# Kernel optimization log

Hardware: AMD Instinct MI355X
Metric: run time of the kernel (lower is better)

Reference implementation:

```python
import jax, jax.numpy as jnp
import numpy as np

EPS = 1e-5

def setup_inputs() -> dict:
    key = jax.random.key(0)
    ks = jax.random.split(key, 5)
    B, C, N, L = 32, 128, 4096, 6
    M = N // 8  # 512
    x = jax.random.normal(ks[0], (B, C, N, 1), dtype=jnp.float32)
    # small init scale keeps softmax logits in a sane range
    W_pool = jax.random.normal(ks[1], (M, C), dtype=jnp.float32) * 0.05
    Wf = jax.random.normal(ks[2], (L, M, M), dtype=jnp.float32) * 0.02
    gamma = jnp.ones((L, M), dtype=jnp.float32)
    beta = jnp.zeros((L, M), dtype=jnp.float32)
    W_unpool = jax.random.normal(ks[3], (M, C), dtype=jnp.float32) * 0.05
    b_unpool = jnp.zeros((M,), dtype=jnp.float32)
    return {"x": x, "W_pool": W_pool, "Wf": Wf, "gamma": gamma,
            "beta": beta, "W_unpool": W_unpool, "b_unpool": b_unpool}


def reference(x, W_pool, Wf, gamma, beta, W_unpool, b_unpool):
    # x: [B, C, N, 1]
    xs = x[..., 0]  # [B, C, N]
    # ---- Pool_1_to_1: 1x1 conv C->M, softmax over N, weighted sum ----
    Spool = jax.nn.softmax(jnp.einsum('mc,bcn->bmn', W_pool, xs), axis=2)
    h = jnp.einsum('bcn,bmn->bmc', xs, Spool)  # pooled then transposed: [B, M, C]
    # ---- n_layers of Order_Aware_Filtering_1_to_1 on [B, M, C] (channels=M) ----
    L = Wf.shape[0]
    for l in range(L):
        y = jnp.einsum('om,bmc->boc', Wf[l], h)  # 1x1 conv M->M
        mu = jnp.mean(y, axis=(0, 2), keepdims=True)          # BN over (B, spatial)
        var = jnp.mean((y - mu) ** 2, axis=(0, 2), keepdims=True)  # biased var
        yn = (y - mu) * jax.lax.rsqrt(var + EPS)
        yn = yn * gamma[l][None, :, None] + beta[l][None, :, None]
        h = jax.nn.relu(yn + h)  # residual + non-lin
    x1 = jnp.transpose(h, (0, 2, 1))  # [B, C, M]
    # ---- Unpool_1_to_1: 1x1 conv (with bias) C->M, softmax over M ----
    ul = jnp.einsum('mc,bcn->bmn', W_unpool, xs) + b_unpool[None, :, None]
    Sun = jax.nn.softmax(ul, axis=1)
    out = jnp.einsum('bcm,bmn->bcn', x1, Sun)
    return out[..., None]  # [B, C, N, 1]
```

## Files before the change

### kernel.cpp

```cpp
#include <hip/hip_runtime.h>
#include <hip/hip_bf16.h>

typedef float f32x4 __attribute__((ext_vector_type(4)));
typedef __bf16 bf16_t;
typedef __bf16 bf16x4 __attribute__((ext_vector_type(4)));
typedef __bf16 bf16x8 __attribute__((ext_vector_type(8)));

#define MFMA16(a, b, c) __builtin_amdgcn_mfma_f32_16x16x32_bf16(a, b, c, 0, 0, 0)

constexpr int C_ = 128;
constexpr int N_ = 4096;
constexpr int M_ = 512;
constexpr int NL = 6;

#define NEG_INF (-__builtin_huge_valf())

constexpr int XST = 136;
constexpr int NSTP = 40;
constexpr int PSTU = 72;

__global__ __launch_bounds__(256) void k_wsplit(const float* __restrict__ W,
                                                bf16_t* __restrict__ hi,
                                                bf16_t* __restrict__ lo) {
  const size_t i4 = ((size_t)blockIdx.x * 256 + threadIdx.x) * 4;
  f32x4 v = *(const f32x4*)&W[i4];
  bf16x4 h4, l4;
#pragma unroll
  for (int k = 0; k < 4; ++k) {
    bf16_t h = (bf16_t)v[k];
    h4[k] = h;
    l4[k] = (bf16_t)(v[k] - (float)h);
  }
  *(bf16x4*)&hi[i4] = h4;
  *(bf16x4*)&lo[i4] = l4;
}

__global__ __launch_bounds__(256) void k_wfsplit(const float* __restrict__ W,
                                                 bf16_t* __restrict__ hi,
                                                 bf16_t* __restrict__ lo) {
  const size_t i4 = ((size_t)blockIdx.x * 256 + threadIdx.x) * 4;
  const int l = (int)(i4 >> 18);
  const int rem = (int)(i4 & 262143);
  const int o = rem >> 9, m = rem & 511;
  f32x4 v = *(const f32x4*)&W[i4];
  bf16x4 h4, l4;
#pragma unroll
  for (int k = 0; k < 4; ++k) {
    bf16_t h = (bf16_t)v[k];
    h4[k] = h;
    l4[k] = (bf16_t)(v[k] - (float)h);
  }
  const size_t ad = (((size_t)l * 16 + (m >> 5)) * 512 + o) * 32 + (m & 31);
  *(bf16x4*)&hi[ad] = h4;
  *(bf16x4*)&lo[ad] = l4;
}

__global__ __launch_bounds__(256) void k_wusplit(const float* __restrict__ W,
                                                 bf16_t* __restrict__ hi,
                                                 bf16_t* __restrict__ lo) {
  const size_t i4 = ((size_t)blockIdx.x * 256 + threadIdx.x) * 4;
  const int m = (int)(i4 >> 7), c = (int)(i4 & 127);
  f32x4 v = *(const f32x4*)&W[i4];
  bf16x4 h4, l4;
#pragma unroll
  for (int k = 0; k < 4; ++k) {
    bf16_t h = (bf16_t)v[k];
    h4[k] = h;
    l4[k] = (bf16_t)(v[k] - (float)h);
  }
  const size_t ad = ((size_t)(c >> 5) * 512 + m) * 32 + (c & 31);
  *(bf16x4*)&hi[ad] = h4;
  *(bf16x4*)&lo[ad] = l4;
}

__global__ __launch_bounds__(256) void k_xsplit(const float* __restrict__ xs,
                                                bf16_t* __restrict__ thi,
                                                bf16_t* __restrict__ tlo) {
  __shared__ float T[128 * 68];
  const int n0 = blockIdx.x * 64, b = blockIdx.y;
  const int t = threadIdx.x;
  const float* xsb = xs + (size_t)b * C_ * N_;
#pragma unroll
  for (int i = 0; i < 8; ++i) {
    int slot = i * 256 + t;
    int c = slot >> 4, n4 = (slot & 15) * 4;
    *(f32x4*)&T[c * 68 + n4] = *(const f32x4*)&xsb[(size_t)c * N_ + n0 + n4];
  }
  __syncthreads();
  const int n = t >> 2, cb = (t & 3) * 32;
  bf16x8 h8[4], l8[4];
#pragma unroll
  for (int g = 0; g < 4; ++g)
#pragma unroll
    for (int j = 0; j < 8; ++j) {
      float v = T[(cb + g * 8 + j) * 68 + n];
      bf16_t hh = (bf16_t)v;
      h8[g][j] = hh;
      l8[g][j] = (bf16_t)(v - (float)hh);
    }
  const size_t base = ((size_t)b * N_ + n0 + n) * C_ + cb;
#pragma unroll
  for (int g = 0; g < 4; ++g) {
    *(bf16x8*)&thi[base + g * 8] = h8[g];
    *(bf16x8*)&tlo[base + g * 8] = l8[g];
  }
}

__global__ __launch_bounds__(256) void k_pool(const bf16_t* __restrict__ xsThi,
                                              const bf16_t* __restrict__ xsTlo,
                                              const float* __restrict__ x,
                                              const bf16_t* __restrict__ Wph,
                                              const bf16_t* __restrict__ Wpl,
                                              float* __restrict__ h_part,
                                              float* __restrict__ ml) {
  __shared__ bf16_t XH2[2][32 * XST], XL2[2][32 * XST];
  __shared__ bf16_t XCH2[2][128 * NSTP], XCL2[2][128 * NSTP];
  const int d = blockIdx.x;
  const int lin = ((d & 7) << 7) | (d >> 3);
  const int b = lin >> 5, r5 = lin & 31;
  const int mt = r5 >> 2, seg = r5 & 3;
  const int m0 = mt * 64;
  const int t = threadIdx.x, w = t >> 6, lane = t & 63, l15 = lane & 15, q = lane >> 4;

  const int sn0 = t >> 4, sn1 = (256 + t) >> 4;
  const int scg = (t & 15) * 8;
  const size_t sgb = ((size_t)b * N_ + seg * 1024) * C_ + scg;
  const int xc2 = t >> 2, xn8 = (t & 3) * 8;
  const float* xb = x + (size_t)b * C_ * N_;

  bf16x8 aWh[4], aWl[4];
#pragma unroll
  for (int k = 0; k < 4; ++k) {
    const size_t ra = (size_t)(m0 + w * 16 + l15) * C_ + k * 32 + q * 8;
    aWh[k] = *(const bf16x8*)&Wph[ra];
    aWl[k] = *(const bf16x8*)&Wpl[ra];
  }

  f32x4 acc[8];
#pragma unroll
  for (int cs = 0; cs < 8; ++cs) acc[cs] = f32x4{0.f, 0.f, 0.f, 0.f};
  float lsum = 0.f;

  bf16x8 th0, th1, tl0, tl1;
  float xf[2][8];

  {
    const size_t off = sgb;
    th0 = *(const bf16x8*)&xsThi[off + (size_t)sn0 * C_];
    th1 = *(const bf16x8*)&xsThi[off + (size_t)sn1 * C_];
    tl0 = *(const bf16x8*)&xsTlo[off + (size_t)sn0 * C_];
    tl1 = *(const bf16x8*)&xsTlo[off + (size_t)sn1 * C_];
#pragma unroll
    for (int i = 0; i < 2; ++i) {
      const int c = xc2 + i * 64;
      *(f32x4*)&xf[i][0] = *(const f32x4*)&xb[(size_t)c * N_ + seg * 1024 + xn8];
      *(f32x4*)&xf[i][4] = *(const f32x4*)&xb[(size_t)c * N_ + seg * 1024 + xn8 + 4];
    }
    *(bf16x8*)&XH2[0][sn0 * XST + scg] = th0;
    *(bf16x8*)&XH2[0][sn1 * XST + scg] = th1;
    *(bf16x8*)&XL2[0][sn0 * XST + scg] = tl0;
    *(bf16x8*)&XL2[0][sn1 * XST + scg] = tl1;
#pragma unroll
    for (int i = 0; i < 2; ++i) {
      const int c = xc2 + i * 64;
      bf16x8 h8, l8;
#pragma unroll
      for (int j = 0; j < 8; ++j) {
        bf16_t hh = (bf16_t)xf[i][j];
        h8[j] = hh;
        l8[j] = (bf16_t)(xf[i][j] - (float)hh);
      }
      *(bf16x8*)&XCH2[0][c * NSTP + xn8] = h8;
      *(bf16x8*)&XCL2[0][c * NSTP + xn8] = l8;
    }
  }

  int p = 0;
  for (int ch = 0; ch < 32; ++ch) {
    __syncthreads();

    if (ch < 31) {
      const int nn = seg * 1024 + (ch + 1) * 32;
      const size_t off = sgb + (size_t)(ch + 1) * 32 * C_;
      th0 = *(const bf16x8*)&xsThi[off + (size_t)sn0 * C_];
      th1 = *(const bf16x8*)&xsThi[off + (size_t)sn1 * C_];
      tl0 = *(const bf16x8*)&xsTlo[off + (size_t)sn0 * C_];
      tl1 = *(const bf16x8*)&xsTlo[off + (size_t)sn1 * C_];
#pragma unroll
      for (int i = 0; i < 2; ++i) {
        const int c = xc2 + i * 64;
        *(f32x4*)&xf[i][0] = *(const f32x4*)&xb[(size_t)c * N_ + nn + xn8];
        *(f32x4*)&xf[i][4] = *(const f32x4*)&xb[(size_t)c * N_ + nn + xn8 + 4];
      }
    }

    const bf16_t* XH = &XH2[p][0];
    const bf16_t* XL = &XL2[p][0];
    const bf16_t* XCH = &XCH2[p][0];
    const bf16_t* XCL = &XCL2[p][0];

    f32x4 U0 = f32x4{0.f, 0.f, 0.f, 0.f}, U1 = f32x4{0.f, 0.f, 0.f, 0.f};
#pragma unroll
    for (int k = 0; k < 4; ++k) {
      {
        const int o = l15 * XST + k * 32 + q * 8;
        bf16x8 bh = *(const bf16x8*)&XH[o];
        bf16x8 bl = *(const bf16x8*)&XL[o];
        U0 = MFMA16(bh, aWh[k], U0);
        U0 = MFMA16(bl, aWh[k], U0);
        U0 = MFMA16(bh, aWl[k], U0);
      }
      {
        const int o = (16 + l15) * XST + k * 32 + q * 8;
        bf16x8 bh = *(const bf16x8*)&XH[o];
        bf16x8 bl = *(const bf16x8*)&XL[o];
        U1 = MFMA16(bh, aWh[k], U1);
        U1 = MFMA16(bl, aWh[k], U1);
        U1 = MFMA16(bh, aWl[k], U1);
      }
    }

    f32x4 pe0, pe1;
#pragma unroll
    for (int r = 0; r < 4; ++r) {
      pe0[r] = __expf(U0[r]);
      pe1[r] = __expf(U1[r]);
      lsum += pe0[r] + pe1[r];
    }

    const int slo = l15 + ((lane & 16) ? 32 : 0);
    float pj[8];
#pragma unroll
    for (int r = 0; r < 4; ++r) {
      float a0 = __shfl(pe0[r], slo);
      float a1 = __shfl(pe1[r], slo);
      pj[r] = (q & 2) ? a1 : a0;
      float b0 = __shfl(pe0[r], slo + 16);
      float b1 = __shfl(pe1[r], slo + 16);
      pj[4 + r] = (q & 2) ? b1 : b0;
    }
    bf16x8 aPh, aPl;
#pragma unroll
    for (int j = 0; j < 8; ++j) {
      bf16_t hh = (bf16_t)pj[j];
      aPh[j] = hh;
      aPl[j] = (bf16_t)(pj[j] - (float)hh);
    }

#pragma unroll
    for (int cs = 0; cs < 8; ++cs) {
      const int ob = (cs * 16 + l15) * NSTP + q * 8;
      bf16x8 bh = *(const bf16x8*)&XCH[ob];
      bf16x8 bl = *(const bf16x8*)&XCL[ob];
      acc[cs] = MFMA16(aPh, bh, acc[cs]);
      acc[cs] = MFMA16(aPh, bl, acc[cs]);
      acc[cs] = MFMA16(aPl, bh, acc[cs]);
    }

    if (ch < 31) {
      const int pn = p ^ 1;
      *(bf16x8*)&XH2[pn][sn0 * XST + scg] = th0;
      *(bf16x8*)&XH2[pn][sn1 * XST + scg] = th1;
      *(bf16x8*)&XL2[pn][sn0 * XST + scg] = tl0;
      *(bf16x8*)&XL2[pn][sn1 * XST + scg] = tl1;
#pragma unroll
      for (int i = 0; i < 2; ++i) {
        const int c = xc2 + i * 64;
        bf16x8 h8, l8;
#pragma unroll
        for (int j = 0; j < 8; ++j) {
          bf16_t hh = (bf16_t)xf[i][j];
          h8[j] = hh;
          l8[j] = (bf16_t)(xf[i][j] - (float)hh);
        }
        *(bf16x8*)&XCH2[pn][c * NSTP + xn8] = h8;
        *(bf16x8*)&XCL2[pn][c * NSTP + xn8] = l8;
      }
    }
    p ^= 1;
  }

  const size_t sb = (size_t)seg * 32 + b;
  lsum += __shfl_xor(lsum, 16);
  lsum += __shfl_xor(lsum, 32);
  if (lane < 16) ml[sb * 512 + m0 + w * 16 + lane] = lsum;
#pragma unroll
  for (int cs = 0; cs < 8; ++cs)
#pragma unroll
    for (int r = 0; r < 4; ++r) {
      const int m = m0 + w * 16 + q * 4 + r;
      h_part[(sb * 512 + m) * 128 + cs * 16 + l15] = acc[cs][r];
    }
}

__global__ __launch_bounds__(128) void k_combine(const float* __restrict__ h_part,
                                                 const float* __restrict__ ml,
                                                 float* __restrict__ hbuf) {
  const int mb = blockIdx.x;
  const int m = mb >> 5, b = mb & 31;
  const int c = threadIdx.x;
  float L = 0.f, acc = 0.f;
#pragma unroll
  for (int s = 0; s < 4; ++s) {
    L += ml[((size_t)s * 32 + b) * 512 + m];
    acc += h_part[(((size_t)s * 32 + b) * 512 + m) * 128 + c];
  }
  hbuf[(size_t)m * 4096 + b * 128 + c] = acc / L;
}

__global__ __launch_bounds__(256) void k_hsplit(const float* __restrict__ h,
                                                bf16_t* __restrict__ thi,
                                                bf16_t* __restrict__ tlo) {
  __shared__ float T[64 * 65];
  const int m0 = blockIdx.x * 64, c0 = blockIdx.y * 64;
  const int t = threadIdx.x;
#pragma unroll
  for (int ii = 0; ii < 4; ++ii) {
    int slot = ii * 256 + t;
    int m = slot >> 4, c4 = (slot & 15) * 4;
    f32x4 v = *(const f32x4*)&h[(size_t)(m0 + m) * 4096 + c0 + c4];
#pragma unroll
    for (int k = 0; k < 4; ++k) T[(c4 + k) * 65 + m] = v[k];
  }
  __syncthreads();
  const int row = t >> 2, mg = (t & 3) * 16;
  const int bc = c0 + row, bb = bc >> 7, cc = bc & 127;
#pragma unroll
  for (int half = 0; half < 2; ++half) {
    bf16x8 h8, l8;
#pragma unroll
    for (int j = 0; j < 8; ++j) {
      float v = T[row * 65 + mg + half * 8 + j];
      bf16_t hh = (bf16_t)v;
      h8[j] = hh;
      l8[j] = (bf16_t)(v - (float)hh);
    }
    const int m8 = m0 + mg + half * 8;
    const size_t ad = (((size_t)bb * 16 + (m8 >> 5)) * 128 + cc) * 32 + (m8 & 31);
    *(bf16x8*)&thi[ad] = h8;
    *(bf16x8*)&tlo[ad] = l8;
  }
}

__global__ __launch_bounds__(256) void k_bnsplit(const float* __restrict__ ybuf,
                                                 float* __restrict__ hbuf,
                                                 const float* __restrict__ stats,
                                                 const float* __restrict__ gamma,
                                                 const float* __restrict__ beta,
                                                 int l,
                                                 bf16_t* __restrict__ thi,
                                                 bf16_t* __restrict__ tlo) {
  __shared__ float T[64 * 65];
  const int m0 = blockIdx.x * 64, c0 = blockIdx.y * 64;
  const int t = threadIdx.x;
#pragma unroll
  for (int ii = 0; ii < 4; ++ii) {
    int slot = ii * 256 + t;
    int m = slot >> 4, c4 = (slot & 15) * 4;
    const int o = m0 + m;
    const float mu = stats[l * 1024 + o] * (1.f / 4096.f);
    const float var = stats[l * 1024 + 512 + o] * (1.f / 4096.f) - mu * mu;
    const float rs = rsqrtf(var + 1e-5f);
    const float g = gamma[l * 512 + o];
    const float bt = beta[l * 512 + o];
    const size_t gidx = (size_t)o * 4096 + c0 + c4;
    f32x4 y = *(const f32x4*)&ybuf[gidx];
    f32x4 h = *(const f32x4*)&hbuf[gidx];
    f32x4 r;
#pragma unroll
    for (int k = 0; k < 4; ++k) {
      r[k] = fmaxf((y[k] - mu) * rs * g + bt + h[k], 0.f);
      T[(c4 + k) * 65 + m] = r[k];
    }
    *(f32x4*)&hbuf[gidx] = r;
  }
  __syncthreads();
  const int row = t >> 2, mg = (t & 3) * 16;
  const int bc = c0 + row, bb = bc >> 7, cc = bc & 127;
#pragma unroll
  for (int half = 0; half < 2; ++half) {
    bf16x8 h8, l8;
#pragma unroll
    for (int j = 0; j < 8; ++j) {
      float v = T[row * 65 + mg + half * 8 + j];
      bf16_t hh = (bf16_t)v;
      h8[j] = hh;
      l8[j] = (bf16_t)(v - (float)hh);
    }
    const int m8 = m0 + mg + half * 8;
    const size_t ad = (((size_t)bb * 16 + (m8 >> 5)) * 128 + cc) * 32 + (m8 & 31);
    *(bf16x8*)&thi[ad] = h8;
    *(bf16x8*)&tlo[ad] = l8;
  }
}

__global__ __launch_bounds__(256) void k_layerA(const bf16_t* __restrict__ Whi,
                                                const bf16_t* __restrict__ Wlo,
                                                const bf16_t* __restrict__ hThi,
                                                const bf16_t* __restrict__ hTlo,
                                                int l, float* __restrict__ ybuf,
                                                float* __restrict__ stats) {
  const int o0 = blockIdx.x * 32;
  const int bb = blockIdx.y;
  const int t = threadIdx.x;
  const int w = t >> 6, lane = t & 63, l15 = lane & 15, q = lane >> 4;
  const int bcw = bb * 128 + w * 32;

  f32x4 acc[2][2];
#pragma unroll
  for (int i = 0; i < 2; ++i)
#pragma unroll
    for (int j = 0; j < 2; ++j) acc[i][j] = f32x4{0.f, 0.f, 0.f, 0.f};

  for (int k0 = 0; k0 < M_; k0 += 32) {
    const int mb = k0 >> 5;
    bf16x8 ah[2], al[2], bh[2], bl[2];
#pragma unroll
    for (int os = 0; os < 2; ++os) {
      const size_t ro =
          (((size_t)l * 16 + mb) * 512 + o0 + os * 16 + l15) * 32 + q * 8;
      ah[os] = *(const bf16x8*)&Whi[ro];
      al[os] = *(const bf16x8*)&Wlo[ro];
    }
#pragma unroll
    for (int ns = 0; ns < 2; ++ns) {
      const size_t rb =
          (((size_t)bb * 16 + mb) * 128 + w * 32 + ns * 16 + l15) * 32 + q * 8;
      bh[ns] = *(const bf16x8*)&hThi[rb];
      bl[ns] = *(const bf16x8*)&hTlo[rb];
    }
#pragma unroll
    for (int os = 0; os < 2; ++os)
#pragma unroll
      for (int ns = 0; ns < 2; ++ns) {
        acc[os][ns] = MFMA16(ah[os], bh[ns], acc[os][ns]);
        acc[os][ns] = MFMA16(ah[os], bl[ns], acc[os][ns]);
        acc[os][ns] = MFMA16(al[os], bh[ns], acc[os][ns]);
      }
  }

  float s1[2][4], s2[2][4];
#pragma unroll
  for (int os = 0; os < 2; ++os)
#pragma unroll
    for (int r = 0; r < 4; ++r) {
      float a = 0.f, b2 = 0.f;
#pragma unroll
      for (int ns = 0; ns < 2; ++ns) {
        float v = acc[os][ns][r];
        ybuf[(size_t)(o0 + os * 16 + q * 4 + r) * 4096 + bcw + ns * 16 + l15] = v;
        a += v;
        b2 += v * v;
      }
      s1[os][r] = a;
      s2[os][r] = b2;
    }
#pragma unroll
  for (int os = 0; os < 2; ++os)
#pragma unroll
    for (int r = 0; r < 4; ++r) {
#pragma unroll
      for (int off = 1; off < 16; off <<= 1) {
        s1[os][r] += __shfl_xor(s1[os][r], off);
        s2[os][r] += __shfl_xor(s2[os][r], off);
      }
      if (l15 == 0) {
        const int o = o0 + os * 16 + q * 4 + r;
        atomicAdd(&stats[l * 1024 + o], s1[os][r]);
        atomicAdd(&stats[l * 1024 + 512 + o], s2[os][r]);
      }
    }
}

__global__ __launch_bounds__(256) void k_unpool(const bf16_t* __restrict__ xsThi,
                                                const bf16_t* __restrict__ xsTlo,
                                                const bf16_t* __restrict__ Wuh,
                                                const bf16_t* __restrict__ Wul,
                                                const float* __restrict__ bun,
                                                const bf16_t* __restrict__ x1hi,
                                                const bf16_t* __restrict__ x1lo,
                                                float* __restrict__ out) {
  __shared__ bf16_t XH[64 * XST], XL[64 * XST];
  __shared__ bf16_t PH2[2][64 * PSTU], PL2[2][64 * PSTU];
  __shared__ float colsum_s[4][64];
  __shared__ float L_s[64];
  const int n0 = blockIdx.x * 64, b = blockIdx.y;
  const int t = threadIdx.x, w = t >> 6, lane = t & 63, l15 = lane & 15, q = lane >> 4;

#pragma unroll
  for (int i = 0; i < 4; ++i) {
    int slot = i * 256 + t;
    int n = slot >> 4, cg = (slot & 15) * 8;
    const size_t g = ((size_t)b * N_ + n0 + n) * C_ + cg;
    *(bf16x8*)&XH[n * XST + cg] = *(const bf16x8*)&xsThi[g];
    *(bf16x8*)&XL[n * XST + cg] = *(const bf16x8*)&xsTlo[g];
  }
  colsum_s[w][lane] = 0.f;
  f32x4 acc[2][4];
#pragma unroll
  for (int cs = 0; cs < 2; ++cs)
#pragma unroll
    for (int nt = 0; nt < 4; ++nt) acc[cs][nt] = f32x4{0.f, 0.f, 0.f, 0.f};
  __syncthreads();

  int p = 0;
  for (int ch = 0; ch < 8; ++ch) {
    const int mg0 = ch * 64 + w * 16;

    bf16x8 xah[2][2], xal[2][2];
#pragma unroll
    for (int ks = 0; ks < 2; ++ks)
#pragma unroll
      for (int cs = 0; cs < 2; ++cs) {
        const size_t ga =
            (((size_t)b * 16 + ch * 2 + ks) * 128 + w * 32 + cs * 16 + l15) * 32 +
            q * 8;
        xah[ks][cs] = *(const bf16x8*)&x1hi[ga];
        xal[ks][cs] = *(const bf16x8*)&x1lo[ga];
      }

    f32x4 U[4];
#pragma unroll
    for (int nt = 0; nt < 4; ++nt) U[nt] = f32x4{0.f, 0.f, 0.f, 0.f};
#pragma unroll
    for (int k = 0; k < 4; ++k) {
      const size_t ra = ((size_t)k * 512 + mg0 + l15) * 32 + q * 8;
      bf16x8 ah = *(const bf16x8*)&Wuh[ra];
      bf16x8 al = *(const bf16x8*)&Wul[ra];
#pragma unroll
      for (int nt = 0; nt < 4; ++nt) {
        const int o = (nt * 16 + l15) * XST + k * 32 + q * 8;
        bf16x8 bh = *(const bf16x8*)&XH[o];
        bf16x8 bl = *(const bf16x8*)&XL[o];
        U[nt] = MFMA16(ah, bh, U[nt]);
        U[nt] = MFMA16(ah, bl, U[nt]);
        U[nt] = MFMA16(al, bh, U[nt]);
      }
    }
    float bi[4];
#pragma unroll
    for (int r = 0; r < 4; ++r) bi[r] = bun[mg0 + q * 4 + r];

#pragma unroll
    for (int nt = 0; nt < 4; ++nt) {
      bf16x4 ph4, pl4;
      float s = 0.f;
#pragma unroll
      for (int r = 0; r < 4; ++r) {
        float pv = __expf(U[nt][r] + bi[r]);
        s += pv;
        bf16_t hh = (bf16_t)pv;
        ph4[r] = hh;
        pl4[r] = (bf16_t)(pv - (float)hh);
      }
      s += __shfl_xor(s, 16);
      s += __shfl_xor(s, 32);
      if (lane < 16) colsum_s[w][nt * 16 + lane] += s;
      const int o = (nt * 16 + l15) * PSTU + w * 16 + q * 4;
      *(bf16x4*)&PH2[p][o] = ph4;
      *(bf16x4*)&PL2[p][o] = pl4;
    }
    __syncthreads();

#pragma unroll
    for (int ks = 0; ks < 2; ++ks) {
#pragma unroll
      for (int nt = 0; nt < 4; ++nt) {
        const int o = (nt * 16 + l15) * PSTU + ks * 32 + q * 8;
        bf16x8 bh = *(const bf16x8*)&PH2[p][o];
        bf16x8 bl = *(const bf16x8*)&PL2[p][o];
#pragma unroll
        for (int cs = 0; cs < 2; ++cs) {
          acc[cs][nt] = MFMA16(xah[ks][cs], bh, acc[cs][nt]);
          acc[cs][nt] = MFMA16(xah[ks][cs], bl, acc[cs][nt]);
          acc[cs][nt] = MFMA16(xal[ks][cs], bh, acc[cs][nt]);
        }
      }
    }
    p ^= 1;
  }
  __syncthreads();
  if (t < 64)
    L_s[t] = colsum_s[0][t] + colsum_s[1][t] + colsum_s[2][t] + colsum_s[3][t];
  __syncthreads();
#pragma unroll
  for (int nt = 0; nt < 4; ++nt) {
    const float invL = 1.f / L_s[nt * 16 + l15];
#pragma unroll
    for (int cs = 0; cs < 2; ++cs) {
      const int c = w * 32 + cs * 16 + q * 4;
#pragma unroll
      for (int r = 0; r < 4; ++r)
        out[((size_t)b * 128 + c + r) * (size_t)N_ + n0 + nt * 16 + l15] =
            acc[cs][nt][r] * invL;
    }
  }
}

extern "C" void kernel_launch(void* const* d_in, const int* in_sizes, int n_in,
                              void* d_out, int out_size, void* d_ws, size_t ws_size,
                              hipStream_t stream) {
  const float* x = (const float*)d_in[0];
  const float* W_pool = (const float*)d_in[1];
  const float* Wf = (const float*)d_in[2];
  const float* gamma = (const float*)d_in[3];
  const float* beta = (const float*)d_in[4];
  const float* W_unpool = (const float*)d_in[5];
  const float* b_unpool = (const float*)d_in[6];
  float* out = (float*)d_out;

  char* ws = (char*)d_ws;
  float* h_part = (float*)ws; ws += (size_t)4 * 32 * 512 * 128 * 4;
  float* ml = (float*)ws;     ws += (size_t)4 * 32 * 512 * 4;
  float* hbuf = (float*)ws;   ws += (size_t)512 * 4096 * 4;
  float* stats = (float*)ws;  ws += NL * 1024 * 4;
  bf16_t* xsThi = (bf16_t*)ws; ws += (size_t)32 * N_ * C_ * 2;
  bf16_t* xsTlo = (bf16_t*)ws; ws += (size_t)32 * N_ * C_ * 2;
  bf16_t* Wuh = (bf16_t*)ws;  ws += (size_t)M_ * C_ * 2;
  bf16_t* Wul = (bf16_t*)ws;  ws += (size_t)M_ * C_ * 2;
  bf16_t* Wph = (bf16_t*)ws;  ws += (size_t)M_ * C_ * 2;
  bf16_t* Wpl = (bf16_t*)ws;  ws += (size_t)M_ * C_ * 2;
  bf16_t* Whi = (bf16_t*)ws;  ws += (size_t)NL * M_ * M_ * 2;
  bf16_t* Wlo = (bf16_t*)ws;  ws += (size_t)NL * M_ * M_ * 2;
  char* hp = (char*)h_part;
  float* ybuf = (float*)(hp);
  bf16_t* hThi = (bf16_t*)(hp + 8388608);
  bf16_t* hTlo = (bf16_t*)(hp + 12582912);

  hipMemsetAsync(stats, 0, NL * 1024 * 4, stream);
  k_xsplit<<<dim3(64, 32), 256, 0, stream>>>(x, xsThi, xsTlo);
  k_wsplit<<<dim3(64), 256, 0, stream>>>(W_pool, Wph, Wpl);
  k_wusplit<<<dim3(64), 256, 0, stream>>>(W_unpool, Wuh, Wul);
  k_wfsplit<<<dim3(1536), 256, 0, stream>>>(Wf, Whi, Wlo);
  k_pool<<<dim3(1024), 256, 0, stream>>>(xsThi, xsTlo, x, Wph, Wpl,
                                         h_part, ml);
  k_combine<<<dim3(16384), 128, 0, stream>>>(h_part, ml, hbuf);
  k_hsplit<<<dim3(8, 64), 256, 0, stream>>>(hbuf, hThi, hTlo);
  for (int l = 0; l < NL; ++l) {
    k_layerA<<<dim3(16, 32), 256, 0, stream>>>(Whi, Wlo, hThi, hTlo, l, ybuf, stats);
    k_bnsplit<<<dim3(8, 64), 256, 0, stream>>>(ybuf, hbuf, stats, gamma, beta, l,
                                               hThi, hTlo);
  }
  k_unpool<<<dim3(64, 32), 256, 0, stream>>>(xsThi, xsTlo, Wuh, Wul, b_unpool,
                                             hThi, hTlo, out);
}
```

Before: 663.9 us.

## Precompute blocked bf16 hi/lo split of x for pool B-operand

k_xsplit now also writes a second hi/lo bf16 copy of x in a [b][n-block][c][32] layout. k_pool reads the MFMA B fragments directly from global memory instead of loading fp32 x, splitting it per block, and staging it through shared memory. This removes the repeated split work, the fp32 loads and the LDS traffic inside the pool loop. In exchange the split kernel writes an extra 64 MB or so, and the MFMA operands are now unstaged global loads on the critical path.

```diff
diff --git a/kernel.cpp b/kernel.cpp
--- a/kernel.cpp
+++ b/kernel.cpp
@@ -16,7 +16,6 @@
 #define NEG_INF (-__builtin_huge_valf())
 
 constexpr int XST = 136;
-constexpr int NSTP = 40;
 constexpr int PSTU = 72;
 
 __global__ __launch_bounds__(256) void k_wsplit(const float* __restrict__ W,
@@ -75,7 +74,9 @@
 
 __global__ __launch_bounds__(256) void k_xsplit(const float* __restrict__ xs,
                                                 bf16_t* __restrict__ thi,
-                                                bf16_t* __restrict__ tlo) {
+                                                bf16_t* __restrict__ tlo,
+                                                bf16_t* __restrict__ bhi,
+                                                bf16_t* __restrict__ blo) {
   __shared__ float T[128 * 68];
   const int n0 = blockIdx.x * 64, b = blockIdx.y;
   const int t = threadIdx.x;
@@ -87,34 +88,56 @@
     *(f32x4*)&T[c * 68 + n4] = *(const f32x4*)&xsb[(size_t)c * N_ + n0 + n4];
   }
   __syncthreads();
-  const int n = t >> 2, cb = (t & 3) * 32;
-  bf16x8 h8[4], l8[4];
-#pragma unroll
-  for (int g = 0; g < 4; ++g)
-#pragma unroll
-    for (int j = 0; j < 8; ++j) {
-      float v = T[(cb + g * 8 + j) * 68 + n];
-      bf16_t hh = (bf16_t)v;
-      h8[g][j] = hh;
-      l8[g][j] = (bf16_t)(v - (float)hh);
-    }
-  const size_t base = ((size_t)b * N_ + n0 + n) * C_ + cb;
-#pragma unroll
-  for (int g = 0; g < 4; ++g) {
-    *(bf16x8*)&thi[base + g * 8] = h8[g];
-    *(bf16x8*)&tlo[base + g * 8] = l8[g];
+  {
+    const int n = t >> 2, cb = (t & 3) * 32;
+    bf16x8 h8[4], l8[4];
+#pragma unroll
+    for (int g = 0; g < 4; ++g)
+#pragma unroll
+      for (int j = 0; j < 8; ++j) {
+        float v = T[(cb + g * 8 + j) * 68 + n];
+        bf16_t hh = (bf16_t)v;
+        h8[g][j] = hh;
+        l8[g][j] = (bf16_t)(v - (float)hh);
+      }
+    const size_t base = ((size_t)b * N_ + n0 + n) * C_ + cb;
+#pragma unroll
+    for (int g = 0; g < 4; ++g) {
+      *(bf16x8*)&thi[base + g * 8] = h8[g];
+      *(bf16x8*)&tlo[base + g * 8] = l8[g];
+    }
+  }
+  {
+    const int half = t >> 7, c = t & 127;
+    const int nb = (n0 >> 5) + half;
+    bf16x8 h8[4], l8[4];
+#pragma unroll
+    for (int g = 0; g < 4; ++g)
+#pragma unroll
+      for (int j = 0; j < 8; ++j) {
+        float v = T[c * 68 + half * 32 + g * 8 + j];
+        bf16_t hh = (bf16_t)v;
+        h8[g][j] = hh;
+        l8[g][j] = (bf16_t)(v - (float)hh);
+      }
+    const size_t base = (((size_t)b * 128 + nb) * 128 + c) * 32;
+#pragma unroll
+    for (int g = 0; g < 4; ++g) {
+      *(bf16x8*)&bhi[base + g * 8] = h8[g];
+      *(bf16x8*)&blo[base + g * 8] = l8[g];
+    }
   }
 }
 
 __global__ __launch_bounds__(256) void k_pool(const bf16_t* __restrict__ xsThi,
                                               const bf16_t* __restrict__ xsTlo,
-                                              const float* __restrict__ x,
+                                              const bf16_t* __restrict__ xsbhi,
+                                              const bf16_t* __restrict__ xsblo,
                                               const bf16_t* __restrict__ Wph,
                                               const bf16_t* __restrict__ Wpl,
                                               float* __restrict__ h_part,
                                               float* __restrict__ ml) {
   __shared__ bf16_t XH2[2][32 * XST], XL2[2][32 * XST];
-  __shared__ bf16_t XCH2[2][128 * NSTP], XCL2[2][128 * NSTP];
   const int d = blockIdx.x;
   const int lin = ((d & 7) << 7) | (d >> 3);
   const int b = lin >> 5, r5 = lin & 31;
@@ -125,8 +148,6 @@
   const int sn0 = t >> 4, sn1 = (256 + t) >> 4;
   const int scg = (t & 15) * 8;
   const size_t sgb = ((size_t)b * N_ + seg * 1024) * C_ + scg;
-  const int xc2 = t >> 2, xn8 = (t & 3) * 8;
-  const float* xb = x + (size_t)b * C_ * N_;
 
   bf16x8 aWh[4], aWl[4];
 #pragma unroll
@@ -142,37 +163,16 @@
   float lsum = 0.f;
 
   bf16x8 th0, th1, tl0, tl1;
-  float xf[2][8];
 
   {
-    const size_t off = sgb;
-    th0 = *(const bf16x8*)&xsThi[off + (size_t)sn0 * C_];
-    th1 = *(const bf16x8*)&xsThi[off + (size_t)sn1 * C_];
-    tl0 = *(const bf16x8*)&xsTlo[off + (size_t)sn0 * C_];
-    tl1 = *(const bf16x8*)&xsTlo[off + (size_t)sn1 * C_];
-#pragma unroll
-    for (int i = 0; i < 2; ++i) {
-      const int c = xc2 + i * 64;
-      *(f32x4*)&xf[i][0] = *(const f32x4*)&xb[(size_t)c * N_ + seg * 1024 + xn8];
-      *(f32x4*)&xf[i][4] = *(const f32x4*)&xb[(size_t)c * N_ + seg * 1024 + xn8 + 4];
-    }
+    th0 = *(const bf16x8*)&xsThi[sgb + (size_t)sn0 * C_];
+    th1 = *(const bf16x8*)&xsThi[sgb + (size_t)sn1 * C_];
+    tl0 = *(const bf16x8*)&xsTlo[sgb + (size_t)sn0 * C_];
+    tl1 = *(const bf16x8*)&xsTlo[sgb + (size_t)sn1 * C_];
     *(bf16x8*)&XH2[0][sn0 * XST + scg] = th0;
     *(bf16x8*)&XH2[0][sn1 * XST + scg] = th1;
     *(bf16x8*)&XL2[0][sn0 * XST + scg] = tl0;
     *(bf16x8*)&XL2[0][sn1 * XST + scg] = tl1;
-#pragma unroll
-    for (int i = 0; i < 2; ++i) {
-      const int c = xc2 + i * 64;
-      bf16x8 h8, l8;
-#pragma unroll
-      for (int j = 0; j < 8; ++j) {
-        bf16_t hh = (bf16_t)xf[i][j];
-        h8[j] = hh;
-        l8[j] = (bf16_t)(xf[i][j] - (float)hh);
-      }
-      *(bf16x8*)&XCH2[0][c * NSTP + xn8] = h8;
-      *(bf16x8*)&XCL2[0][c * NSTP + xn8] = l8;
-    }
   }
 
   int p = 0;
@@ -180,24 +180,15 @@
     __syncthreads();
 
     if (ch < 31) {
-      const int nn = seg * 1024 + (ch + 1) * 32;
       const size_t off = sgb + (size_t)(ch + 1) * 32 * C_;
       th0 = *(const bf16x8*)&xsThi[off + (size_t)sn0 * C_];
       th1 = *(const bf16x8*)&xsThi[off + (size_t)sn1 * C_];
       tl0 = *(const bf16x8*)&xsTlo[off + (size_t)sn0 * C_];
       tl1 = *(const bf16x8*)&xsTlo[off + (size_t)sn1 * C_];
-#pragma unroll
-      for (int i = 0; i < 2; ++i) {
-        const int c = xc2 + i * 64;
-        *(f32x4*)&xf[i][0] = *(const f32x4*)&xb[(size_t)c * N_ + nn + xn8];
-        *(f32x4*)&xf[i][4] = *(const f32x4*)&xb[(size_t)c * N_ + nn + xn8 + 4];
-      }
     }
 
     const bf16_t* XH = &XH2[p][0];
     const bf16_t* XL = &XL2[p][0];
-    const bf16_t* XCH = &XCH2[p][0];
-    const bf16_t* XCL = &XCL2[p][0];
 
     f32x4 U0 = f32x4{0.f, 0.f, 0.f, 0.f}, U1 = f32x4{0.f, 0.f, 0.f, 0.f};
 #pragma unroll
@@ -247,11 +238,12 @@
       aPl[j] = (bf16_t)(pj[j] - (float)hh);
     }
 
+    const size_t abase = (((size_t)b * 128 + seg * 32 + ch) * 128) * 32;
 #pragma unroll
     for (int cs = 0; cs < 8; ++cs) {
-      const int ob = (cs * 16 + l15) * NSTP + q * 8;
-      bf16x8 bh = *(const bf16x8*)&XCH[ob];
-      bf16x8 bl = *(const bf16x8*)&XCL[ob];
+      const size_t gb = abase + (size_t)(cs * 16 + l15) * 32 + q * 8;
+      bf16x8 bh = *(const bf16x8*)&xsbhi[gb];
+      bf16x8 bl = *(const bf16x8*)&xsblo[gb];
       acc[cs] = MFMA16(aPh, bh, acc[cs]);
       acc[cs] = MFMA16(aPh, bl, acc[cs]);
       acc[cs] = MFMA16(aPl, bh, acc[cs]);
@@ -263,19 +255,6 @@
       *(bf16x8*)&XH2[pn][sn1 * XST + scg] = th1;
       *(bf16x8*)&XL2[pn][sn0 * XST + scg] = tl0;
       *(bf16x8*)&XL2[pn][sn1 * XST + scg] = tl1;
-#pragma unroll
-      for (int i = 0; i < 2; ++i) {
-        const int c = xc2 + i * 64;
-        bf16x8 h8, l8;
-#pragma unroll
-        for (int j = 0; j < 8; ++j) {
-          bf16_t hh = (bf16_t)xf[i][j];
-          h8[j] = hh;
-          l8[j] = (bf16_t)(xf[i][j] - (float)hh);
-        }
-        *(bf16x8*)&XCH2[pn][c * NSTP + xn8] = h8;
-        *(bf16x8*)&XCL2[pn][c * NSTP + xn8] = l8;
-      }
     }
     p ^= 1;
   }
@@ -616,6 +595,8 @@
   float* stats = (float*)ws;  ws += NL * 1024 * 4;
   bf16_t* xsThi = (bf16_t*)ws; ws += (size_t)32 * N_ * C_ * 2;
   bf16_t* xsTlo = (bf16_t*)ws; ws += (size_t)32 * N_ * C_ * 2;
+  bf16_t* xsbhi = (bf16_t*)ws; ws += (size_t)32 * N_ * C_ * 2;
+  bf16_t* xsblo = (bf16_t*)ws; ws += (size_t)32 * N_ * C_ * 2;
   bf16_t* Wuh = (bf16_t*)ws;  ws += (size_t)M_ * C_ * 2;
   bf16_t* Wul = (bf16_t*)ws;  ws += (size_t)M_ * C_ * 2;
   bf16_t* Wph = (bf16_t*)ws;  ws += (size_t)M_ * C_ * 2;
@@ -628,11 +609,11 @@
   bf16_t* hTlo = (bf16_t*)(hp + 12582912);
 
   hipMemsetAsync(stats, 0, NL * 1024 * 4, stream);
-  k_xsplit<<<dim3(64, 32), 256, 0, stream>>>(x, xsThi, xsTlo);
+  k_xsplit<<<dim3(64, 32), 256, 0, stream>>>(x, xsThi, xsTlo, xsbhi, xsblo);
   k_wsplit<<<dim3(64), 256, 0, stream>>>(W_pool, Wph, Wpl);
   k_wusplit<<<dim3(64), 256, 0, stream>>>(W_unpool, Wuh, Wul);
   k_wfsplit<<<dim3(1536), 256, 0, stream>>>(Wf, Whi, Wlo);
-  k_pool<<<dim3(1024), 256, 0, stream>>>(xsThi, xsTlo, x, Wph, Wpl,
+  k_pool<<<dim3(1024), 256, 0, stream>>>(xsThi, xsTlo, xsbhi, xsblo, Wph, Wpl,
                                          h_part, ml);
   k_combine<<<dim3(16384), 128, 0, stream>>>(h_part, ml, hbuf);
   k_hsplit<<<dim3(8, 64), 256, 0, stream>>>(hbuf, hThi, hTlo);
```

Result: slower. 759.6 us (+14.4%).
